# Optimization experiments

Hardware: AMD Instinct MI355X
Metric: run time of the kernel (lower is better)

## Reference

```python
import jax, jax.numpy as jnp
import numpy as np

N = 100000   # nodes
E = 1600000  # edges
D_IN = 256
H = 64       # hidden_dim


def _segment_softmax(e, dst, n):
    # e: [E, heads]; softmax over edges sharing the same dst node
    m = jax.ops.segment_max(e, dst, num_segments=n)
    m = jnp.where(jnp.isfinite(m), m, jnp.zeros_like(m))
    ex = jnp.exp(e - m[dst])
    s = jax.ops.segment_sum(ex, dst, num_segments=n)
    return ex / (s[dst] + 1e-16)


def gat_conv(x, edge_index, W, att_src, att_dst, bias, heads, odim):
    # PyG GATConv, concat=False (mean over heads), with self-loops, neg_slope=0.2
    n = x.shape[0]
    loop = jnp.arange(n, dtype=edge_index.dtype)
    src = jnp.concatenate([edge_index[0], loop])
    dst = jnp.concatenate([edge_index[1], loop])
    h = (x @ W).reshape(n, heads, odim)                      # [N, heads, odim]
    a_s = jnp.einsum('nhd,hd->nh', h, att_src)               # [N, heads]
    a_d = jnp.einsum('nhd,hd->nh', h, att_dst)
    e = jax.nn.leaky_relu(a_s[src] + a_d[dst], 0.2)          # [E+N, heads]
    alpha = _segment_softmax(e, dst, n)
    msg = h[src] * alpha[:, :, None]                         # gather + weight
    out = jax.ops.segment_sum(msg, dst, num_segments=n)      # scatter-reduce
    return out.mean(axis=1) + bias                           # concat=False -> mean


def gcn_conv(x, edge_index, W, bias):
    # PyG GCNConv with self-loops and symmetric normalization
    n = x.shape[0]
    loop = jnp.arange(n, dtype=edge_index.dtype)
    src = jnp.concatenate([edge_index[0], loop])
    dst = jnp.concatenate([edge_index[1], loop])
    deg = jax.ops.segment_sum(jnp.ones(src.shape[0], x.dtype), dst, num_segments=n)
    dinv = jnp.where(deg > 0, deg ** -0.5, jnp.zeros_like(deg))
    norm = dinv[src] * dinv[dst]                             # [E+N]
    h = x @ W
    return jax.ops.segment_sum(h[src] * norm[:, None], dst, num_segments=n) + bias


def setup_inputs() -> dict:
    key = jax.random.key(0)
    ks = jax.random.split(key, 16)
    f = lambda k, shp, s=0.05: (jax.random.normal(k, shp, dtype=jnp.float32) * s)
    inp = {
        'x': jax.random.normal(ks[0], (N, D_IN), dtype=jnp.float32),
        'edge_index': jax.random.randint(ks[1], (2, E), 0, N, dtype=jnp.int64),
        # GAT layer 1: heads=4, out=H
        'W1': f(ks[2], (D_IN, 4 * H)), 'a1s': f(ks[3], (4, H)), 'a1d': f(ks[4], (4, H)),
        'b1': jnp.zeros((H,), jnp.float32),
        # GAT layer 2: heads=2, out=H
        'W2': f(ks[5], (H, 2 * H)), 'a2s': f(ks[6], (2, H)), 'a2d': f(ks[7], (2, H)),
        'b2': jnp.zeros((H,), jnp.float32),
        # GCN layer: H -> H//2
        'Wg': f(ks[8], (H, H // 2)), 'bg': jnp.zeros((H // 2,), jnp.float32),
        # MLP head: H//2 -> H//4 -> 1
        'Wh1': f(ks[9], (H // 2, H // 4)), 'bh1': jnp.zeros((H // 4,), jnp.float32),
        'Wh2': f(ks[10], (H // 4, 1)), 'bh2': jnp.zeros((1,), jnp.float32),
    }
    return inp


def reference(x, edge_index, W1, a1s, a1d, b1, W2, a2s, a2d, b2, Wg, bg, Wh1, bh1, Wh2, bh2):
    h1 = jax.nn.relu(gat_conv(x, edge_index, W1, a1s, a1d, b1, heads=4, odim=H))
    h2 = jax.nn.relu(gat_conv(h1, edge_index, W2, a2s, a2d, b2, heads=2, odim=H))
    h3 = jax.nn.relu(gcn_conv(h2, edge_index, Wg, bg))
    z = jax.nn.relu(h3 @ Wh1 + bh1)
    svi = jax.nn.sigmoid(z @ Wh2 + bh2)
    return svi.squeeze(-1)
```

## Files before the change

kernel.cpp:

```cpp
#include <hip/hip_runtime.h>
#include <math.h>

static inline int cdiv(int a, int b){ return (a + b - 1) / b; }

typedef __attribute__((ext_vector_type(8))) short short8_t;
typedef __attribute__((ext_vector_type(4))) float f32x4;
typedef __attribute__((ext_vector_type(2))) float f32x2;

static __device__ inline unsigned short f2bf(float f) {
    union { float f; unsigned u; } v; v.f = f;
    unsigned r = v.u + 0x7fff + ((v.u >> 16) & 1);
    return (unsigned short)(r >> 16);
}

static __device__ inline unsigned char f2fp8(float f) {
    union { float f; unsigned u; } v; v.f = f;
    unsigned s = (v.u >> 24) & 0x80u;
    v.u &= 0x7fffffffu;
    v.f = fminf(v.f, 448.f);
    unsigned out;
    if (v.u >= (121u << 23)) {
        unsigned u = v.u + 0x7FFFFu + ((v.u >> 20) & 1u);
        out = (((u >> 23) - 120u) << 3) | ((u >> 20) & 7u);
    } else {
        out = (unsigned)(v.f * 512.f + 0.5f);
    }
    return (unsigned char)(out | s);
}

static __device__ inline float fp8_1(unsigned b) {
    unsigned s = (b & 0x80u) << 24;
    unsigned em = b & 0x7fu;
    union { unsigned u; float f; } n;
    n.u = (((em >> 3) + 120u) << 23) | ((em & 7u) << 20);
    float mag = (em >= 8u) ? n.f : (float)em * 0.001953125f;
    union { unsigned u; float f; } r; r.f = mag; r.u |= s;
    return r.f;
}

static __device__ __forceinline__ f32x2 fp8lo(unsigned v) {
#if __has_builtin(__builtin_amdgcn_cvt_pk_f32_fp8)
    return __builtin_amdgcn_cvt_pk_f32_fp8((int)v, false);
#else
    f32x2 r; r[0] = fp8_1(v & 0xff); r[1] = fp8_1((v >> 8) & 0xff); return r;
#endif
}
static __device__ __forceinline__ f32x2 fp8hi(unsigned v) {
#if __has_builtin(__builtin_amdgcn_cvt_pk_f32_fp8)
    return __builtin_amdgcn_cvt_pk_f32_fp8((int)v, true);
#else
    f32x2 r; r[0] = fp8_1((v >> 16) & 0xff); r[1] = fp8_1(v >> 24); return r;
#endif
}


__global__ void k_count_deg(const int* __restrict__ dst, int E, int* __restrict__ deg) {
    int base = (blockIdx.x * 256 + threadIdx.x) * 4;
    if (base + 3 < E) {
        int4 d = *(const int4*)(dst + base);
        atomicAdd(&deg[d.x], 1); atomicAdd(&deg[d.y], 1);
        atomicAdd(&deg[d.z], 1); atomicAdd(&deg[d.w], 1);
    } else {
        for (int k = 0; k < 4; k++)
            if (base + k < E) atomicAdd(&deg[dst[base + k]], 1);
    }
}

__global__ void k_scan_partial(const int* __restrict__ deg, int n, int* __restrict__ partial) {
    __shared__ int sd[256];
    int base = blockIdx.x * 1024;
    int sum = 0;
    for (int i = threadIdx.x; i < 1024; i += 256) {
        int idx = base + i;
        if (idx < n) sum += deg[idx] + 1;
    }
    sd[threadIdx.x] = sum;
    __syncthreads();
    for (int s = 128; s > 0; s >>= 1) {
        if (threadIdx.x < s) sd[threadIdx.x] += sd[threadIdx.x + s];
        __syncthreads();
    }
    if (threadIdx.x == 0) partial[blockIdx.x] = sd[0];
}

__global__ void k_scan_top(int* __restrict__ partial, int nb, int* __restrict__ offs, int n) {
    if (blockIdx.x == 0 && threadIdx.x == 0) {
        int run = 0;
        for (int i = 0; i < nb; i++) { int v = partial[i]; partial[i] = run; run += v; }
        offs[n] = run;
    }
}

__global__ void k_scan_final(const int* __restrict__ deg, int n,
                             const int* __restrict__ partial, int* __restrict__ offs,
                             int* __restrict__ cursor, int* __restrict__ csr,
                             float* __restrict__ dinv) {
    __shared__ int sd[256];
    int tid = threadIdx.x;
    int base = blockIdx.x * 1024;
    int v[4]; int s0 = 0;
    #pragma unroll
    for (int j = 0; j < 4; j++) {
        int idx = base + tid*4 + j;
        v[j] = (idx < n) ? (deg[idx] + 1) : 0;
        s0 += v[j];
    }
    sd[tid] = s0;
    __syncthreads();
    for (int st = 1; st < 256; st <<= 1) {
        int t = (tid >= st) ? sd[tid - st] : 0;
        __syncthreads();
        sd[tid] += t;
        __syncthreads();
    }
    int ex = (tid > 0 ? sd[tid - 1] : 0) + partial[blockIdx.x];
    #pragma unroll
    for (int j = 0; j < 4; j++) {
        int idx = base + tid*4 + j;
        if (idx < n) {
            offs[idx]   = ex;
            cursor[idx] = ex;
            dinv[idx]   = rsqrtf((float)v[j]);
            csr[ex + v[j] - 1] = idx;
        }
        ex += v[j];
    }
}

__global__ __launch_bounds__(256) void k_fill_csr_win(const int* __restrict__ src,
        const int* __restrict__ dst, int E,
        int* __restrict__ cursor, int* __restrict__ csr, int wsize) {
    int win   = blockIdx.x & 7;
    int chunk = blockIdx.x >> 3;
    int lo = win * wsize, hi = lo + wsize;
    int base = (chunk * 256 + threadIdx.x) * 4;
    if (base + 3 < E) {
        int4 d = *(const int4*)(dst + base);
        int4 s = *(const int4*)(src + base);
        if (d.x >= lo && d.x < hi) { int p = atomicAdd(&cursor[d.x], 1); csr[p] = s.x; }
        if (d.y >= lo && d.y < hi) { int p = atomicAdd(&cursor[d.y], 1); csr[p] = s.y; }
        if (d.z >= lo && d.z < hi) { int p = atomicAdd(&cursor[d.z], 1); csr[p] = s.z; }
        if (d.w >= lo && d.w < hi) { int p = atomicAdd(&cursor[d.w], 1); csr[p] = s.w; }
    } else {
        for (int k = 0; k < 4; k++) {
            int e = base + k;
            if (e < E) {
                int d = dst[e];
                if (d >= lo && d < hi) { int p = atomicAdd(&cursor[d], 1); csr[p] = src[e]; }
            }
        }
    }
}


__global__ void k_prep_w1(const float* __restrict__ W, unsigned short* __restrict__ Bt) {
    int t = blockIdx.x * 256 + threadIdx.x;
    int k = t >> 8, c = t & 255;
    Bt[c * 256 + k] = f2bf(W[t]);
}

__global__ __launch_bounds__(512) void k_gemm1_mfma(const float* __restrict__ A,
        const unsigned short* __restrict__ Bt, const float* __restrict__ att_s_g,
        const float* __restrict__ att_d_g, unsigned char* __restrict__ C,
        float* __restrict__ out_as, float* __restrict__ out_ad, int M) {
    constexpr int LDP = 40;
    __shared__ __align__(16) unsigned short As[128 * LDP];
    __shared__ __align__(16) unsigned short Bs[256 * LDP];
    __shared__ float att_l[512];
    int tid = threadIdx.x;
    int bm = blockIdx.x * 128;
    int wave = tid >> 6, lane = tid & 63;
    int wr = wave >> 1, wc = wave & 1;
    int lg = lane >> 4, lr = lane & 15;

    att_l[tid] = (tid < 256) ? att_s_g[tid] : att_d_g[tid - 256];

    f32x4 acc[2][8] = {};

    for (int k0 = 0; k0 < 256; k0 += 32) {
        __syncthreads();
        {
            int row = tid >> 2, part = tid & 3;
            int gr = bm + row;
            float4 v0, v1;
            if (gr < M) {
                const float4* p = (const float4*)(A + (size_t)gr * 256 + k0 + part * 8);
                v0 = p[0]; v1 = p[1];
            } else {
                v0 = make_float4(0.f,0.f,0.f,0.f); v1 = v0;
            }
            unsigned short* w = &As[row * LDP + part * 8];
            w[0]=f2bf(v0.x); w[1]=f2bf(v0.y); w[2]=f2bf(v0.z); w[3]=f2bf(v0.w);
            w[4]=f2bf(v1.x); w[5]=f2bf(v1.y); w[6]=f2bf(v1.z); w[7]=f2bf(v1.w);
        }
        {
            int col = tid >> 1, part = tid & 1;
            const uint4* p = (const uint4*)(Bt + (size_t)col * 256 + k0 + part * 16);
            uint4 u0 = p[0], u1 = p[1];
            *(uint4*)&Bs[col * LDP + part * 16]     = u0;
            *(uint4*)&Bs[col * LDP + part * 16 + 8] = u1;
        }
        __syncthreads();
        short8_t a[2], b[8];
        #pragma unroll
        for (int i = 0; i < 2; i++)
            a[i] = *(const short8_t*)&As[(wr * 32 + i * 16 + lr) * LDP + lg * 8];
        #pragma unroll
        for (int j = 0; j < 8; j++)
            b[j] = *(const short8_t*)&Bs[(wc * 128 + j * 16 + lr) * LDP + lg * 8];
        #pragma unroll
        for (int i = 0; i < 2; i++)
            #pragma unroll
            for (int j = 0; j < 8; j++)
                acc[i][j] = __builtin_amdgcn_mfma_f32_16x16x32_bf16(a[i], b[j], acc[i][j], 0, 0, 0);
    }
    float ws[8], wd[8];
    #pragma unroll
    for (int j = 0; j < 8; j++) {
        int c = wc * 128 + j * 16 + lr;
        ws[j] = att_l[c]; wd[j] = att_l[256 + c];
    }
    #pragma unroll
    for (int i = 0; i < 2; i++) {
        #pragma unroll
        for (int b2 = 0; b2 < 4; b2++) {
            int row = bm + wr * 32 + i * 16 + lg * 4 + b2;
            #pragma unroll
            for (int j = 0; j < 8; j++) {
                int col = wc * 128 + j * 16 + lr;
                if (row < M) C[(size_t)row * 256 + col] = f2fp8(acc[i][j][b2]);
            }
            float s0=0.f, s1=0.f, d0=0.f, d1=0.f;
            #pragma unroll
            for (int j = 0; j < 4; j++) { float v = acc[i][j][b2];   s0 += v*ws[j];   d0 += v*wd[j]; }
            #pragma unroll
            for (int j = 4; j < 8; j++) { float v = acc[i][j][b2];   s1 += v*ws[j];   d1 += v*wd[j]; }
            #pragma unroll
            for (int off = 1; off < 16; off <<= 1) {
                s0 += __shfl_xor(s0, off); s1 += __shfl_xor(s1, off);
                d0 += __shfl_xor(d0, off); d1 += __shfl_xor(d1, off);
            }
            if (lr == 0 && row < M) {
                out_as[row * 4 + wc * 2]     = s0;
                out_as[row * 4 + wc * 2 + 1] = s1;
                out_ad[row * 4 + wc * 2]     = d0;
                out_ad[row * 4 + wc * 2 + 1] = d1;
            }
        }
    }
}


template<int NCB, int NC, bool OB, bool ATT>
__global__ __launch_bounds__(256) void k_gemm_k64(const float* __restrict__ A,
                                                  const float* __restrict__ B,
                                                  const float* __restrict__ att_s_g,
                                                  const float* __restrict__ att_d_g,
                                                  void* __restrict__ Cv,
                                                  float* __restrict__ out_as,
                                                  float* __restrict__ out_ad, int M) {
    constexpr int TN = NCB / 16;
    __shared__ float As[64][65];
    __shared__ float Bs[64][NCB + 1];
    __shared__ float att_l[ATT ? 2 * NCB : 1];
    int tid = threadIdx.x;
    int bm = blockIdx.x * 64;
    int bn = blockIdx.y * NCB;
    if constexpr (ATT) {
        if (tid < 2 * NCB)
            att_l[tid] = (tid < NCB) ? att_s_g[bn + tid] : att_d_g[bn + tid - NCB];
    }
    {
        int c = tid & 63, r0 = tid >> 6;
        #pragma unroll
        for (int it = 0; it < 16; it++) {
            int r = r0 + it * 4;
            int gr = bm + r;
            As[r][c] = (gr < M) ? A[(size_t)gr * 64 + c] : 0.f;
        }
    }
    for (int i = tid; i < 64 * NCB; i += 256) {
        int r = i / NCB, cc = i % NCB;
        Bs[r][cc] = B[(size_t)r * NC + bn + cc];
    }
    __syncthreads();
    int ty = tid >> 4, tx = tid & 15;
    float acc[4][TN] = {};
    #pragma unroll 8
    for (int k = 0; k < 64; k++) {
        float a[4], b[TN];
        #pragma unroll
        for (int i = 0; i < 4; i++) a[i] = As[ty + 16*i][k];
        #pragma unroll
        for (int j = 0; j < TN; j++) b[j] = Bs[k][tx + 16*j];
        #pragma unroll
        for (int i = 0; i < 4; i++)
            #pragma unroll
            for (int j = 0; j < TN; j++) acc[i][j] += a[i] * b[j];
    }
    float ws[TN], wd[TN];
    if constexpr (ATT) {
        #pragma unroll
        for (int j = 0; j < TN; j++) { ws[j] = att_l[tx + 16*j]; wd[j] = att_l[NCB + tx + 16*j]; }
    }
    #pragma unroll
    for (int i = 0; i < 4; i++) {
        int gr = bm + ty + 16*i;
        #pragma unroll
        for (int j = 0; j < TN; j++) {
            if (gr < M) {
                if constexpr (OB)
                    ((unsigned char*)Cv)[(size_t)gr * NC + bn + tx + 16*j] = f2fp8(acc[i][j]);
                else
                    ((float*)Cv)[(size_t)gr * NC + bn + tx + 16*j] = acc[i][j];
            }
        }
        if constexpr (ATT) {
            float s = 0.f, d = 0.f;
            #pragma unroll
            for (int j = 0; j < TN; j++) { s += acc[i][j]*ws[j]; d += acc[i][j]*wd[j]; }
            #pragma unroll
            for (int off = 1; off < 16; off <<= 1) { s += __shfl_xor(s, off); d += __shfl_xor(d, off); }
            if (tx == 0 && gr < M) {
                out_as[gr * 2 + blockIdx.y] = s;
                out_ad[gr * 2 + blockIdx.y] = d;
            }
        }
    }
}


template<int HEADS>
__global__ __launch_bounds__(256) void k_gat_fused(const unsigned char* __restrict__ hpre,
        const float* __restrict__ as_n, const float* __restrict__ ad_n,
        const float* __restrict__ bias,
        const int* __restrict__ offs, const int* __restrict__ csr,
        float* __restrict__ out, int n_nodes) {
    __shared__ int   s_src[4][64];
    __shared__ float s_p[4][64 * HEADS];
    int wif  = threadIdx.x >> 6;
    int lane = threadIdx.x & 63;
    int n = blockIdx.x * 4 + wif;
    if (n >= n_nodes) return;
    const int beg = offs[n];
    const int deg = offs[n + 1] - beg;

    int h_id, dq;
    if constexpr (HEADS == 4) { h_id = lane >> 4; dq = lane & 15; }
    else                      { h_id = lane >> 5; dq = lane & 31; }

    float adv[HEADS];
    if constexpr (HEADS == 4) {
        float4 t = *(const float4*)(ad_n + (size_t)n * 4);
        adv[0]=t.x; adv[1]=t.y; adv[2]=t.z; adv[3]=t.w;
    } else {
        float2 t = *(const float2*)(ad_n + (size_t)n * 2);
        adv[0]=t.x; adv[1]=t.y;
    }

    float sumh = 0.f;
    float acc[HEADS] = {};

    for (int j0 = 0; j0 < deg; j0 += 64) {
        int j = j0 + lane;
        int cnt = min(64, deg - j0);
        if (j < deg) {
            int s = csr[beg + j];
            s_src[wif][lane] = s;
            float ev[HEADS];
            if constexpr (HEADS == 4) {
                float4 t = *(const float4*)(as_n + (size_t)s * 4);
                ev[0]=t.x; ev[1]=t.y; ev[2]=t.z; ev[3]=t.w;
            } else {
                float2 t = *(const float2*)(as_n + (size_t)s * 2);
                ev[0]=t.x; ev[1]=t.y;
            }
            #pragma unroll
            for (int h = 0; h < HEADS; h++) {
                float e = ev[h] + adv[h];
                e = fmaxf(e, 0.2f * e);
                s_p[wif][lane * HEADS + h] = __expf(e);
            }
        }
        #pragma unroll 4
        for (int q = 0; q < cnt; q++) {
            int s = s_src[wif][q];
            float p = s_p[wif][q * HEADS + h_id];
            sumh += p;
            if constexpr (HEADS == 4) {
                unsigned v = *(const unsigned*)(hpre + (size_t)s * 256 + h_id * 64 + dq * 4);
                f32x2 l = fp8lo(v), h2 = fp8hi(v);
                acc[0] += p * l[0]; acc[1] += p * l[1];
                acc[2] += p * h2[0]; acc[3] += p * h2[1];
            } else {
                unsigned v = *(const unsigned short*)(hpre + (size_t)s * 128 + h_id * 64 + dq * 2);
                f32x2 l = fp8lo(v);
                acc[0] += p * l[0]; acc[1] += p * l[1];
            }
        }
    }
    float inv = 1.0f / (sumh + 1e-16f);
    float r[HEADS];
    #pragma unroll
    for (int c = 0; c < HEADS; c++) r[c] = acc[c] * inv;
    if constexpr (HEADS == 4) {
        #pragma unroll
        for (int c = 0; c < 4; c++) {
            r[c] += __shfl_xor(r[c], 16);
            r[c] += __shfl_xor(r[c], 32);
            r[c] *= 0.25f;
        }
        if (h_id == 0) {
            float4 b = *(const float4*)(bias + dq * 4);
            float4 o;
            o.x = fmaxf(r[0] + b.x, 0.f); o.y = fmaxf(r[1] + b.y, 0.f);
            o.z = fmaxf(r[2] + b.z, 0.f); o.w = fmaxf(r[3] + b.w, 0.f);
            *(float4*)(out + (size_t)n * 64 + dq * 4) = o;
        }
    } else {
        #pragma unroll
        for (int c = 0; c < 2; c++) {
            r[c] += __shfl_xor(r[c], 32);
            r[c] *= 0.5f;
        }
        if (h_id == 0) {
            float2 b = *(const float2*)(bias + dq * 2);
            float2 o;
            o.x = fmaxf(r[0] + b.x, 0.f); o.y = fmaxf(r[1] + b.y, 0.f);
            *(float2*)(out + (size_t)n * 64 + dq * 2) = o;
        }
    }
}


__global__ __launch_bounds__(256) void k_gcn_agg(const unsigned char* __restrict__ hpre,
        const float* __restrict__ dinv, const float* __restrict__ bias,
        const int* __restrict__ offs, const int* __restrict__ csr,
        float* __restrict__ out, int n_nodes) {
    int gid = blockIdx.x * 256 + threadIdx.x;
    int n = gid >> 3, q = gid & 7;
    if (n >= n_nodes) return;
    const int beg = offs[n], end = offs[n + 1];
    float4 acc = make_float4(0.f,0.f,0.f,0.f);
    #pragma unroll 4
    for (int j = beg; j < end; j++) {
        int s = csr[j];
        float ds = dinv[s];
        unsigned v = *(const unsigned*)(hpre + (size_t)s * 32 + q * 4);
        f32x2 l = fp8lo(v), h2 = fp8hi(v);
        acc.x += ds * l[0]; acc.y += ds * l[1];
        acc.z += ds * h2[0]; acc.w += ds * h2[1];
    }
    float dn = dinv[n];
    float4 b = *(const float4*)(bias + q * 4);
    float4 o;
    o.x = fmaxf(acc.x * dn + b.x, 0.f); o.y = fmaxf(acc.y * dn + b.y, 0.f);
    o.z = fmaxf(acc.z * dn + b.z, 0.f); o.w = fmaxf(acc.w * dn + b.w, 0.f);
    *(float4*)(out + (size_t)n * 32 + q * 4) = o;
}


__global__ __launch_bounds__(256) void k_mlp(const float* __restrict__ h3,
        const float* __restrict__ Wh1, const float* __restrict__ bh1,
        const float* __restrict__ Wh2, const float* __restrict__ bh2,
        float* __restrict__ out, int n_nodes) {
    __shared__ float w1[512];
    __shared__ float w2[16];
    __shared__ float b1s[16];
    __shared__ float b2s;
    int tid = threadIdx.x;
    for (int i = tid; i < 512; i += 256) w1[i] = Wh1[i];
    if (tid < 16) { w2[tid] = Wh2[tid]; b1s[tid] = bh1[tid]; }
    if (tid == 0) b2s = bh2[0];
    __syncthreads();
    int n = blockIdx.x * 256 + tid;
    if (n >= n_nodes) return;
    float x[32];
    const float4* p = (const float4*)(h3 + (size_t)n * 32);
    #pragma unroll
    for (int q = 0; q < 8; q++) { float4 v = p[q]; x[4*q] = v.x; x[4*q+1] = v.y; x[4*q+2] = v.z; x[4*q+3] = v.w; }
    float acc2 = b2s;
    #pragma unroll
    for (int j = 0; j < 16; j++) {
        float z = b1s[j];
        #pragma unroll
        for (int k = 0; k < 32; k++) z += x[k] * w1[k * 16 + j];
        z = fmaxf(z, 0.f);
        acc2 += z * w2[j];
    }
    out[n] = 1.0f / (1.0f + expf(-acc2));
}


extern "C" void kernel_launch(void* const* d_in, const int* in_sizes, int n_in,
                              void* d_out, int out_size, void* d_ws, size_t ws_size,
                              hipStream_t stream) {
    const float* x   = (const float*)d_in[0];
    const int*   ei  = (const int*)d_in[1];
    const float* W1  = (const float*)d_in[2];
    const float* a1s = (const float*)d_in[3];
    const float* a1d = (const float*)d_in[4];
    const float* b1  = (const float*)d_in[5];
    const float* W2  = (const float*)d_in[6];
    const float* a2s = (const float*)d_in[7];
    const float* a2d = (const float*)d_in[8];
    const float* b2  = (const float*)d_in[9];
    const float* Wg  = (const float*)d_in[10];
    const float* bg  = (const float*)d_in[11];
    const float* Wh1 = (const float*)d_in[12];
    const float* bh1 = (const float*)d_in[13];
    const float* Wh2 = (const float*)d_in[14];
    const float* bh2 = (const float*)d_in[15];

    const int N = in_sizes[0] / 256;
    const int E = in_sizes[1] / 2;
    const int* srcs = ei;
    const int* dsts = ei + E;

    float* R0   = (float*)d_ws;
    float* R1   = R0 + (size_t)N * 256;
    float* R2   = R1 + (size_t)N * 64;
    float* As_  = R2 + (size_t)N * 64;
    float* Ad_  = As_ + (size_t)N * 4;
    float* dinv = Ad_ + (size_t)N * 4;
    int* deg    = (int*)(dinv + N);
    int* offs   = deg + N;
    int* cursor = offs + (N + 1);
    int* csr    = cursor + N;
    int* parts  = csr + (E + N);
    unsigned short* W1t = (unsigned short*)(parts + 256);
    unsigned char*  HP  = (unsigned char*)R0;

    hipMemsetAsync(deg, 0, (size_t)N * sizeof(int), stream);
    k_count_deg<<<cdiv(E, 1024), 256, 0, stream>>>(dsts, E, deg);
    int nch = cdiv(N, 1024);
    k_scan_partial<<<nch, 256, 0, stream>>>(deg, N, parts);
    k_scan_top<<<1, 64, 0, stream>>>(parts, nch, offs, N);
    k_scan_final<<<nch, 256, 0, stream>>>(deg, N, parts, offs, cursor, csr, dinv);
    int wsize = cdiv(N, 8);
    k_fill_csr_win<<<cdiv(E, 1024) * 8, 256, 0, stream>>>(srcs, dsts, E, cursor, csr, wsize);

    k_prep_w1<<<256, 256, 0, stream>>>(W1, W1t);
    k_gemm1_mfma<<<cdiv(N, 128), 512, 0, stream>>>(x, W1t, a1s, a1d, HP, As_, Ad_, N);
    k_gat_fused<4><<<cdiv(N, 4), 256, 0, stream>>>(HP, As_, Ad_, b1, offs, csr, R1, N);

    dim3 g2(cdiv(N, 64), 2);
    k_gemm_k64<64, 128, true, true><<<g2, 256, 0, stream>>>(R1, W2, a2s, a2d, HP, As_, Ad_, N);
    k_gat_fused<2><<<cdiv(N, 4), 256, 0, stream>>>(HP, As_, Ad_, b2, offs, csr, R2, N);

    dim3 g3(cdiv(N, 64), 1);
    k_gemm_k64<32, 32, true, false><<<g3, 256, 0, stream>>>(R2, Wg, nullptr, nullptr, HP, nullptr, nullptr, N);
    k_gcn_agg<<<cdiv(N * 8, 256), 256, 0, stream>>>(HP, dinv, bg, offs, csr, R1, N);

    k_mlp<<<cdiv(N, 256), 256, 0, stream>>>(R1, Wh1, bh1, Wh2, bh2, (float*)d_out, N);
}
```

Baseline: 449.8 us.

## Use bf16 MFMA for small GEMMs, windowed degree count, wider GAT gathers

Replaces the scalar-FMA layer-2 and GCN GEMMs with a bf16 MFMA kernel that uses pre-transposed bf16 weights, with the attention dot products fused into the epilogue. Degree counting now runs in 8 destination windows to localize atomics, and the CSR fill skips the src load when no edge in the group falls in the window. The GAT aggregation is restructured so each lane loads 8 fp8 values per edge and several edges are processed in parallel per wave, followed by cross-lane reductions. The GEMM inputs are rounded to bf16, which adds some precision loss.

```diff
diff --git a/kernel.cpp b/kernel.cpp
--- a/kernel.cpp
+++ b/kernel.cpp
@@ -54,15 +54,23 @@
 }
 
 
-__global__ void k_count_deg(const int* __restrict__ dst, int E, int* __restrict__ deg) {
-    int base = (blockIdx.x * 256 + threadIdx.x) * 4;
+__global__ __launch_bounds__(256) void k_count_deg_win(const int* __restrict__ dst, int E,
+        int* __restrict__ deg, int wsize) {
+    int win   = blockIdx.x & 7;
+    int chunk = blockIdx.x >> 3;
+    int lo = win * wsize, hi = lo + wsize;
+    int base = (chunk * 256 + threadIdx.x) * 4;
     if (base + 3 < E) {
         int4 d = *(const int4*)(dst + base);
-        atomicAdd(&deg[d.x], 1); atomicAdd(&deg[d.y], 1);
-        atomicAdd(&deg[d.z], 1); atomicAdd(&deg[d.w], 1);
+        if (d.x >= lo && d.x < hi) atomicAdd(&deg[d.x], 1);
+        if (d.y >= lo && d.y < hi) atomicAdd(&deg[d.y], 1);
+        if (d.z >= lo && d.z < hi) atomicAdd(&deg[d.z], 1);
+        if (d.w >= lo && d.w < hi) atomicAdd(&deg[d.w], 1);
     } else {
-        for (int k = 0; k < 4; k++)
-            if (base + k < E) atomicAdd(&deg[dst[base + k]], 1);
+        for (int k = 0; k < 4; k++) {
+            int e = base + k;
+            if (e < E) { int d = dst[e]; if (d >= lo && d < hi) atomicAdd(&deg[d], 1); }
+        }
     }
 }
 
@@ -136,11 +144,15 @@
     int base = (chunk * 256 + threadIdx.x) * 4;
     if (base + 3 < E) {
         int4 d = *(const int4*)(dst + base);
-        int4 s = *(const int4*)(src + base);
-        if (d.x >= lo && d.x < hi) { int p = atomicAdd(&cursor[d.x], 1); csr[p] = s.x; }
-        if (d.y >= lo && d.y < hi) { int p = atomicAdd(&cursor[d.y], 1); csr[p] = s.y; }
-        if (d.z >= lo && d.z < hi) { int p = atomicAdd(&cursor[d.z], 1); csr[p] = s.z; }
-        if (d.w >= lo && d.w < hi) { int p = atomicAdd(&cursor[d.w], 1); csr[p] = s.w; }
+        bool ix = d.x >= lo && d.x < hi, iy = d.y >= lo && d.y < hi;
+        bool iz = d.z >= lo && d.z < hi, iw = d.w >= lo && d.w < hi;
+        if (ix | iy | iz | iw) {
+            int4 s = *(const int4*)(src + base);
+            if (ix) { int p = atomicAdd(&cursor[d.x], 1); csr[p] = s.x; }
+            if (iy) { int p = atomicAdd(&cursor[d.y], 1); csr[p] = s.y; }
+            if (iz) { int p = atomicAdd(&cursor[d.z], 1); csr[p] = s.z; }
+            if (iw) { int p = atomicAdd(&cursor[d.w], 1); csr[p] = s.w; }
+        }
     } else {
         for (int k = 0; k < 4; k++) {
             int e = base + k;
@@ -153,10 +165,10 @@
 }
 
 
-__global__ void k_prep_w1(const float* __restrict__ W, unsigned short* __restrict__ Bt) {
+__global__ void k_prep_wt(const float* __restrict__ W, unsigned short* __restrict__ Bt,
+                          int K, int C) {
     int t = blockIdx.x * 256 + threadIdx.x;
-    int k = t >> 8, c = t & 255;
-    Bt[c * 256 + k] = f2bf(W[t]);
+    if (t < K * C) { int k = t / C, c = t % C; Bt[c * K + k] = f2bf(W[t]); }
 }
 
 __global__ __launch_bounds__(512) void k_gemm1_mfma(const float* __restrict__ A,
@@ -251,79 +263,84 @@
 }
 
 
-template<int NCB, int NC, bool OB, bool ATT>
-__global__ __launch_bounds__(256) void k_gemm_k64(const float* __restrict__ A,
-                                                  const float* __restrict__ B,
-                                                  const float* __restrict__ att_s_g,
-                                                  const float* __restrict__ att_d_g,
-                                                  void* __restrict__ Cv,
-                                                  float* __restrict__ out_as,
-                                                  float* __restrict__ out_ad, int M) {
-    constexpr int TN = NCB / 16;
-    __shared__ float As[64][65];
-    __shared__ float Bs[64][NCB + 1];
-    __shared__ float att_l[ATT ? 2 * NCB : 1];
+template<int NC, bool ATT>
+__global__ __launch_bounds__(256) void k_gemm_k64_mfma(const float* __restrict__ A,
+        const unsigned short* __restrict__ Bt,
+        const float* __restrict__ att_s_g, const float* __restrict__ att_d_g,
+        unsigned char* __restrict__ C, float* __restrict__ out_as,
+        float* __restrict__ out_ad, int M) {
+    constexpr int NF  = NC / 16;
+    constexpr int LDP = 72;
+    __shared__ __align__(16) unsigned short As[64 * LDP];
+    __shared__ __align__(16) unsigned short Bs[NC * LDP];
+    __shared__ float att_l[ATT ? 2 * NC : 1];
     int tid = threadIdx.x;
     int bm = blockIdx.x * 64;
-    int bn = blockIdx.y * NCB;
+    int wave = tid >> 6, lane = tid & 63, lg = lane >> 4, lr = lane & 15;
+
     if constexpr (ATT) {
-        if (tid < 2 * NCB)
-            att_l[tid] = (tid < NCB) ? att_s_g[bn + tid] : att_d_g[bn + tid - NCB];
+        if (tid < 2 * NC)
+            att_l[tid] = (tid < NC) ? att_s_g[tid] : att_d_g[tid - NC];
     }
     {
-        int c = tid & 63, r0 = tid >> 6;
-        #pragma unroll
-        for (int it = 0; it < 16; it++) {
-            int r = r0 + it * 4;
-            int gr = bm + r;
-            As[r][c] = (gr < M) ? A[(size_t)gr * 64 + c] : 0.f;
-        }
-    }
-    for (int i = tid; i < 64 * NCB; i += 256) {
-        int r = i / NCB, cc = i % NCB;
-        Bs[r][cc] = B[(size_t)r * NC + bn + cc];
+        int row = tid >> 2, part = tid & 3;
+        int gr = bm + row;
+        float4 v0, v1, v2, v3;
+        if (gr < M) {
+            const float4* p = (const float4*)(A + (size_t)gr * 64 + part * 16);
+            v0 = p[0]; v1 = p[1]; v2 = p[2]; v3 = p[3];
+        } else {
+            v0 = make_float4(0.f,0.f,0.f,0.f); v1 = v0; v2 = v0; v3 = v0;
+        }
+        unsigned short* w = &As[row * LDP + part * 16];
+        w[0]=f2bf(v0.x);  w[1]=f2bf(v0.y);  w[2]=f2bf(v0.z);  w[3]=f2bf(v0.w);
+        w[4]=f2bf(v1.x);  w[5]=f2bf(v1.y);  w[6]=f2bf(v1.z);  w[7]=f2bf(v1.w);
+        w[8]=f2bf(v2.x);  w[9]=f2bf(v2.y);  w[10]=f2bf(v2.z); w[11]=f2bf(v2.w);
+        w[12]=f2bf(v3.x); w[13]=f2bf(v3.y); w[14]=f2bf(v3.z); w[15]=f2bf(v3.w);
+    }
+    for (int i = tid; i < NC * 8; i += 256) {
+        int c = i >> 3, part = i & 7;
+        *(uint4*)&Bs[c * LDP + part * 8] = *(const uint4*)(Bt + (size_t)c * 64 + part * 8);
     }
     __syncthreads();
-    int ty = tid >> 4, tx = tid & 15;
-    float acc[4][TN] = {};
-    #pragma unroll 8
-    for (int k = 0; k < 64; k++) {
-        float a[4], b[TN];
-        #pragma unroll
-        for (int i = 0; i < 4; i++) a[i] = As[ty + 16*i][k];
-        #pragma unroll
-        for (int j = 0; j < TN; j++) b[j] = Bs[k][tx + 16*j];
-        #pragma unroll
-        for (int i = 0; i < 4; i++)
-            #pragma unroll
-            for (int j = 0; j < TN; j++) acc[i][j] += a[i] * b[j];
-    }
-    float ws[TN], wd[TN];
+
+    f32x4 acc[NF] = {};
+    short8_t a0 = *(const short8_t*)&As[(wave * 16 + lr) * LDP + lg * 8];
+    short8_t a1 = *(const short8_t*)&As[(wave * 16 + lr) * LDP + 32 + lg * 8];
+    #pragma unroll
+    for (int j = 0; j < NF; j++) {
+        short8_t b0 = *(const short8_t*)&Bs[(j * 16 + lr) * LDP + lg * 8];
+        short8_t b1 = *(const short8_t*)&Bs[(j * 16 + lr) * LDP + 32 + lg * 8];
+        acc[j] = __builtin_amdgcn_mfma_f32_16x16x32_bf16(a0, b0, acc[j], 0, 0, 0);
+        acc[j] = __builtin_amdgcn_mfma_f32_16x16x32_bf16(a1, b1, acc[j], 0, 0, 0);
+    }
+    float ws[NF], wd[NF];
     if constexpr (ATT) {
         #pragma unroll
-        for (int j = 0; j < TN; j++) { ws[j] = att_l[tx + 16*j]; wd[j] = att_l[NCB + tx + 16*j]; }
-    }
-    #pragma unroll
-    for (int i = 0; i < 4; i++) {
-        int gr = bm + ty + 16*i;
-        #pragma unroll
-        for (int j = 0; j < TN; j++) {
-            if (gr < M) {
-                if constexpr (OB)
-                    ((unsigned char*)Cv)[(size_t)gr * NC + bn + tx + 16*j] = f2fp8(acc[i][j]);
-                else
-                    ((float*)Cv)[(size_t)gr * NC + bn + tx + 16*j] = acc[i][j];
-            }
-        }
+        for (int j = 0; j < NF; j++) { ws[j] = att_l[j * 16 + lr]; wd[j] = att_l[NC + j * 16 + lr]; }
+    }
+    #pragma unroll
+    for (int b2 = 0; b2 < 4; b2++) {
+        int row = bm + wave * 16 + lg * 4 + b2;
+        #pragma unroll
+        for (int j = 0; j < NF; j++)
+            if (row < M) C[(size_t)row * NC + j * 16 + lr] = f2fp8(acc[j][b2]);
         if constexpr (ATT) {
-            float s = 0.f, d = 0.f;
-            #pragma unroll
-            for (int j = 0; j < TN; j++) { s += acc[i][j]*ws[j]; d += acc[i][j]*wd[j]; }
-            #pragma unroll
-            for (int off = 1; off < 16; off <<= 1) { s += __shfl_xor(s, off); d += __shfl_xor(d, off); }
-            if (tx == 0 && gr < M) {
-                out_as[gr * 2 + blockIdx.y] = s;
-                out_ad[gr * 2 + blockIdx.y] = d;
+            float s0=0.f, s1=0.f, d0=0.f, d1=0.f;
+            #pragma unroll
+            for (int j = 0; j < 4; j++) { float v = acc[j][b2]; s0 += v*ws[j]; d0 += v*wd[j]; }
+            #pragma unroll
+            for (int j = 4; j < 8; j++) { float v = acc[j][b2]; s1 += v*ws[j]; d1 += v*wd[j]; }
+            #pragma unroll
+            for (int off = 1; off < 16; off <<= 1) {
+                s0 += __shfl_xor(s0, off); s1 += __shfl_xor(s1, off);
+                d0 += __shfl_xor(d0, off); d1 += __shfl_xor(d1, off);
+            }
+            if (lr == 0 && row < M) {
+                out_as[row * 2]     = s0;
+                out_as[row * 2 + 1] = s1;
+                out_ad[row * 2]     = d0;
+                out_ad[row * 2 + 1] = d1;
             }
         }
     }
@@ -345,9 +362,11 @@
     const int beg = offs[n];
     const int deg = offs[n + 1] - beg;
 
-    int h_id, dq;
-    if constexpr (HEADS == 4) { h_id = lane >> 4; dq = lane & 15; }
-    else                      { h_id = lane >> 5; dq = lane & 31; }
+    constexpr int EPI = (HEADS == 4) ? 2 : 4;
+    int eo, h;
+    if constexpr (HEADS == 4) { eo = lane >> 5; h = (lane >> 3) & 3; }
+    else                      { eo = lane >> 4; h = (lane >> 3) & 1; }
+    int dq8 = lane & 7;
 
     float adv[HEADS];
     if constexpr (HEADS == 4) {
@@ -359,7 +378,7 @@
     }
 
     float sumh = 0.f;
-    float acc[HEADS] = {};
+    float acc[8] = {};
 
     for (int j0 = 0; j0 < deg; j0 += 64) {
         int j = j0 + lane;
@@ -376,59 +395,62 @@
                 ev[0]=t.x; ev[1]=t.y;
             }
             #pragma unroll
-            for (int h = 0; h < HEADS; h++) {
-                float e = ev[h] + adv[h];
+            for (int hh = 0; hh < HEADS; hh++) {
+                float e = ev[hh] + adv[hh];
                 e = fmaxf(e, 0.2f * e);
-                s_p[wif][lane * HEADS + h] = __expf(e);
-            }
-        }
-        #pragma unroll 4
-        for (int q = 0; q < cnt; q++) {
-            int s = s_src[wif][q];
-            float p = s_p[wif][q * HEADS + h_id];
-            sumh += p;
-            if constexpr (HEADS == 4) {
-                unsigned v = *(const unsigned*)(hpre + (size_t)s * 256 + h_id * 64 + dq * 4);
-                f32x2 l = fp8lo(v), h2 = fp8hi(v);
-                acc[0] += p * l[0]; acc[1] += p * l[1];
-                acc[2] += p * h2[0]; acc[3] += p * h2[1];
-            } else {
-                unsigned v = *(const unsigned short*)(hpre + (size_t)s * 128 + h_id * 64 + dq * 2);
-                f32x2 l = fp8lo(v);
-                acc[0] += p * l[0]; acc[1] += p * l[1];
-            }
+                s_p[wif][lane * HEADS + hh] = __expf(e);
+            }
+        }
+        #pragma unroll 2
+        for (int q = 0; q < cnt; q += EPI) {
+            int qe = q + eo;
+            if (qe < cnt) {
+                int s = s_src[wif][qe];
+                float p = s_p[wif][qe * HEADS + h];
+                sumh += p;
+                uint2 v = *(const uint2*)(hpre + (size_t)s * (HEADS * 64) + h * 64 + dq8 * 8);
+                f32x2 c0 = fp8lo(v.x), c1 = fp8hi(v.x), c2 = fp8lo(v.y), c3 = fp8hi(v.y);
+                acc[0] += p * c0[0]; acc[1] += p * c0[1];
+                acc[2] += p * c1[0]; acc[3] += p * c1[1];
+                acc[4] += p * c2[0]; acc[5] += p * c2[1];
+                acc[6] += p * c3[0]; acc[7] += p * c3[1];
+            }
+        }
+    }
+    if constexpr (HEADS == 4) {
+        sumh += __shfl_xor(sumh, 32);
+        #pragma unroll
+        for (int i = 0; i < 8; i++) acc[i] += __shfl_xor(acc[i], 32);
+    } else {
+        sumh += __shfl_xor(sumh, 16); sumh += __shfl_xor(sumh, 32);
+        #pragma unroll
+        for (int i = 0; i < 8; i++) {
+            acc[i] += __shfl_xor(acc[i], 16); acc[i] += __shfl_xor(acc[i], 32);
         }
     }
     float inv = 1.0f / (sumh + 1e-16f);
-    float r[HEADS];
-    #pragma unroll
-    for (int c = 0; c < HEADS; c++) r[c] = acc[c] * inv;
+    float r[8];
+    #pragma unroll
+    for (int i = 0; i < 8; i++) r[i] = acc[i] * inv;
     if constexpr (HEADS == 4) {
         #pragma unroll
-        for (int c = 0; c < 4; c++) {
-            r[c] += __shfl_xor(r[c], 16);
-            r[c] += __shfl_xor(r[c], 32);
-            r[c] *= 0.25f;
-        }
-        if (h_id == 0) {
-            float4 b = *(const float4*)(bias + dq * 4);
-            float4 o;
-            o.x = fmaxf(r[0] + b.x, 0.f); o.y = fmaxf(r[1] + b.y, 0.f);
-            o.z = fmaxf(r[2] + b.z, 0.f); o.w = fmaxf(r[3] + b.w, 0.f);
-            *(float4*)(out + (size_t)n * 64 + dq * 4) = o;
+        for (int i = 0; i < 8; i++) {
+            r[i] += __shfl_xor(r[i], 8); r[i] += __shfl_xor(r[i], 16); r[i] *= 0.25f;
         }
     } else {
         #pragma unroll
-        for (int c = 0; c < 2; c++) {
-            r[c] += __shfl_xor(r[c], 32);
-            r[c] *= 0.5f;
-        }
-        if (h_id == 0) {
-            float2 b = *(const float2*)(bias + dq * 2);
-            float2 o;
-            o.x = fmaxf(r[0] + b.x, 0.f); o.y = fmaxf(r[1] + b.y, 0.f);
-            *(float2*)(out + (size_t)n * 64 + dq * 2) = o;
-        }
+        for (int i = 0; i < 8; i++) { r[i] += __shfl_xor(r[i], 8); r[i] *= 0.5f; }
+    }
+    if (lane < 8) {
+        float4 b0 = *(const float4*)(bias + dq8 * 8);
+        float4 b1 = *(const float4*)(bias + dq8 * 8 + 4);
+        float4 o0, o1;
+        o0.x = fmaxf(r[0] + b0.x, 0.f); o0.y = fmaxf(r[1] + b0.y, 0.f);
+        o0.z = fmaxf(r[2] + b0.z, 0.f); o0.w = fmaxf(r[3] + b0.w, 0.f);
+        o1.x = fmaxf(r[4] + b1.x, 0.f); o1.y = fmaxf(r[5] + b1.y, 0.f);
+        o1.z = fmaxf(r[6] + b1.z, 0.f); o1.w = fmaxf(r[7] + b1.w, 0.f);
+        *(float4*)(out + (size_t)n * 64 + dq8 * 8)     = o0;
+        *(float4*)(out + (size_t)n * 64 + dq8 * 8 + 4) = o1;
     }
 }
 
@@ -529,27 +551,30 @@
     int* csr    = cursor + N;
     int* parts  = csr + (E + N);
     unsigned short* W1t = (unsigned short*)(parts + 256);
+    unsigned short* W2t = W1t + 65536;
+    unsigned short* Wgt = W2t + 8192;
     unsigned char*  HP  = (unsigned char*)R0;
 
+    int wsize = cdiv(N, 8);
     hipMemsetAsync(deg, 0, (size_t)N * sizeof(int), stream);
-    k_count_deg<<<cdiv(E, 1024), 256, 0, stream>>>(dsts, E, deg);
+    k_count_deg_win<<<cdiv(E, 1024) * 8, 256, 0, stream>>>(dsts, E, deg, wsize);
     int nch = cdiv(N, 1024);
     k_scan_partial<<<nch, 256, 0, stream>>>(deg, N, parts);
     k_scan_top<<<1, 64, 0, stream>>>(parts, nch, offs, N);
     k_scan_final<<<nch, 256, 0, stream>>>(deg, N, parts, offs, cursor, csr, dinv);
-    int wsize = cdiv(N, 8);
     k_fill_csr_win<<<cdiv(E, 1024) * 8, 256, 0, stream>>>(srcs, dsts, E, cursor, csr, wsize);
 
-    k_prep_w1<<<256, 256, 0, stream>>>(W1, W1t);
+    k_prep_wt<<<256, 256, 0, stream>>>(W1, W1t, 256, 256);
+    k_prep_wt<<<32, 256, 0, stream>>>(W2, W2t, 64, 128);
+    k_prep_wt<<<8, 256, 0, stream>>>(Wg, Wgt, 64, 32);
+
     k_gemm1_mfma<<<cdiv(N, 128), 512, 0, stream>>>(x, W1t, a1s, a1d, HP, As_, Ad_, N);
     k_gat_fused<4><<<cdiv(N, 4), 256, 0, stream>>>(HP, As_, Ad_, b1, offs, csr, R1, N);
 
-    dim3 g2(cdiv(N, 64), 2);
-    k_gemm_k64<64, 128, true, true><<<g2, 256, 0, stream>>>(R1, W2, a2s, a2d, HP, As_, Ad_, N);
+    k_gemm_k64_mfma<128, true><<<cdiv(N, 64), 256, 0, stream>>>(R1, W2t, a2s, a2d, HP, As_, Ad_, N);
     k_gat_fused<2><<<cdiv(N, 4), 256, 0, stream>>>(HP, As_, Ad_, b2, offs, csr, R2, N);
 
-    dim3 g3(cdiv(N, 64), 1);
-    k_gemm_k64<32, 32, true, false><<<g3, 256, 0, stream>>>(R2, Wg, nullptr, nullptr, HP, nullptr, nullptr, N);
+    k_gemm_k64_mfma<32, false><<<cdiv(N, 64), 256, 0, stream>>>(R2, Wgt, nullptr, nullptr, HP, nullptr, nullptr, N);
     k_gcn_agg<<<cdiv(N * 8, 256), 256, 0, stream>>>(HP, dinv, bg, offs, csr, R1, N);
 
     k_mlp<<<cdiv(N, 256), 256, 0, stream>>>(R1, Wh1, bh1, Wh2, bh2, (float*)d_out, N);
```

Result: faster. 426.2 us (-5.2%).
